# Performance work log

Hardware: AMD Instinct MI355X
Metric: run time of the kernel (lower is better)

Reference implementation:

```python
import jax, jax.numpy as jnp
import numpy as np

HEADS = 8
DIM_HEAD = 32


def setup_inputs() -> dict:
    key = jax.random.key(0)
    k1, k2, k3, k4 = jax.random.split(key, 4)
    dim, hidden = 256, HEADS * DIM_HEAD
    x = jax.random.normal(k1, (4, dim, 48, 48), dtype=jnp.float32)
    # 1x1 conv weights stored as [out_ch, in_ch]
    w_qkv = jax.random.normal(k2, (3 * hidden, dim), dtype=jnp.float32) * (dim ** -0.5)
    w_out = jax.random.normal(k3, (dim, hidden), dtype=jnp.float32) * (hidden ** -0.5)
    b_out = jax.random.normal(k4, (dim,), dtype=jnp.float32) * 0.01
    return {"x": x, "w_qkv": w_qkv, "w_out": w_out, "b_out": b_out}


def reference(x, w_qkv, w_out, b_out):
    B, C, H, W = x.shape
    n = H * W
    scale = DIM_HEAD ** -0.5
    # 1x1 conv QKV projection: [B, 3*hidden, H, W] -> [B, 3, heads, dh, n]
    qkv = jnp.einsum('oc,bchw->bohw', w_qkv, x).reshape(B, 3, HEADS, DIM_HEAD, n)
    q, k, v = qkv[:, 0], qkv[:, 1], qkv[:, 2]  # each [B, h, dh, n]
    sim = jnp.einsum('bhdi,bhdj->bhij', q, k) * scale  # [B, h, n, n]
    attn = jax.nn.softmax(sim, axis=-1)
    out = jnp.einsum('bhij,bhdj->bhdi', attn, v)  # [B, h, dh, n] -> channels (h d)
    out = out.reshape(B, HEADS * DIM_HEAD, H, W)
    return jnp.einsum('oc,bchw->bohw', w_out, out) + b_out[None, :, None, None]
```

## Files before the change

### kernel.cpp

```cpp
#include <hip/hip_runtime.h>
#include <hip/hip_bf16.h>

#define NSP 2304
#define NB  4

typedef unsigned short u16;
typedef __attribute__((ext_vector_type(8))) short short8;
typedef __attribute__((ext_vector_type(4))) float f32x4;
typedef __attribute__((ext_vector_type(4))) unsigned short u16x4;

#define K1S 0.25508040852656425f

static __device__ inline u16 f2bf(float f) {
  return __builtin_bit_cast(unsigned short, __float2bfloat16(f));
}
static __device__ inline unsigned cvtpk(float a, float b) {
  unsigned r;
  asm("v_cvt_pk_bf16_f32 %0, %1, %2" : "=v"(r) : "v"(a), "v"(b));
  return r;
}

__global__ __launch_bounds__(256) void convert_w(
    const float* __restrict__ wq, const float* __restrict__ wo,
    u16* __restrict__ dst) {
  int i = (blockIdx.x * 256 + threadIdx.x) * 4;
  float4 v;
  if (i < 196608) v = *(const float4*)(wq + i);
  else            v = *(const float4*)(wo + (i - 196608));
  u16x4 p = {f2bf(v.x), f2bf(v.y), f2bf(v.z), f2bf(v.w)};
  *(u16x4*)(dst + i) = p;
}

__global__ __launch_bounds__(256) void transpose_x(
    const float* __restrict__ x, u16* __restrict__ xT) {
  __shared__ float tile[32][33];
  const int t = threadIdx.x;
  const int n0 = blockIdx.x * 32, c0 = blockIdx.y * 32, b = blockIdx.z;
  const float* xb = x + ((size_t)b * 256 + c0) * NSP + n0;
#pragma unroll
  for (int e = t; e < 1024; e += 256) {
    int cc = e >> 5, nn = e & 31;
    tile[cc][nn] = xb[(size_t)cc * NSP + nn];
  }
  __syncthreads();
  u16* xTb = xT + ((size_t)b * NSP + n0) * 256 + c0;
#pragma unroll
  for (int e = t; e < 1024; e += 256) {
    int nn = e >> 5, cc = e & 31;
    xTb[(size_t)nn * 256 + cc] = f2bf(tile[cc][nn]);
  }
}

template <int EPI>
__global__ __launch_bounds__(256) void gemm_mfma(
    const u16* __restrict__ A, const u16* __restrict__ B,
    u16* __restrict__ qkT, u16* __restrict__ vbuf,
    float* __restrict__ outf, const float* __restrict__ bias, int N) {
  __shared__ u16 As[64][264];
  __shared__ u16 Bs[64][264];
  const int t = threadIdx.x, lane = t & 63, wid = t >> 6;
  const int lo = lane & 15, g = lane >> 4;
  const int wr = wid >> 1, wc = wid & 1;
  const int row0 = blockIdx.y * 64, col0 = blockIdx.x * 64, b = blockIdx.z;

  const int sr = t >> 2, c4 = t & 3;
  const u16* Arow = A + (size_t)(row0 + sr) * 256;
  const u16* Brow = B + ((size_t)b * N + col0 + sr) * 256;
#pragma unroll
  for (int i = 0; i < 8; ++i) {
    int col = (c4 + 4 * i) * 8;
    *(uint4*)&As[sr][col] = *(const uint4*)&Arow[col];
    *(uint4*)&Bs[sr][col] = *(const uint4*)&Brow[col];
  }
  __syncthreads();

  f32x4 acc[2][2];
#pragma unroll
  for (int i = 0; i < 2; ++i)
#pragma unroll
    for (int j = 0; j < 2; ++j) acc[i][j] = (f32x4){0, 0, 0, 0};

  const int ar0 = wr * 32 + lo, br0 = wc * 32 + lo;
#pragma unroll
  for (int kk = 0; kk < 8; ++kk) {
    int kc = kk * 32 + g * 8;
    short8 a0 = *(const short8*)&As[ar0][kc];
    short8 a1 = *(const short8*)&As[ar0 + 16][kc];
    short8 b0 = *(const short8*)&Bs[br0][kc];
    short8 b1 = *(const short8*)&Bs[br0 + 16][kc];
    acc[0][0] = __builtin_amdgcn_mfma_f32_16x16x32_bf16(a0, b0, acc[0][0], 0, 0, 0);
    acc[0][1] = __builtin_amdgcn_mfma_f32_16x16x32_bf16(a0, b1, acc[0][1], 0, 0, 0);
    acc[1][0] = __builtin_amdgcn_mfma_f32_16x16x32_bf16(a1, b0, acc[1][0], 0, 0, 0);
    acc[1][1] = __builtin_amdgcn_mfma_f32_16x16x32_bf16(a1, b1, acc[1][1], 0, 0, 0);
  }

  const float qs = (EPI == 0 && row0 < 256) ? K1S : 1.0f;
#pragma unroll
  for (int m2 = 0; m2 < 2; ++m2)
#pragma unroll
    for (int n2 = 0; n2 < 2; ++n2) {
      int m = row0 + wr * 32 + m2 * 16 + g * 4;
      int n = col0 + wc * 32 + n2 * 16 + lo;
      if constexpr (EPI == 0) {
        if (row0 < 512) {
          u16x4 pk = {f2bf(acc[m2][n2][0] * qs), f2bf(acc[m2][n2][1] * qs),
                      f2bf(acc[m2][n2][2] * qs), f2bf(acc[m2][n2][3] * qs)};
          *(u16x4*)(qkT + ((size_t)b * NSP + n) * 512 + m) = pk;
        } else {
#pragma unroll
          for (int r = 0; r < 4; ++r)
            vbuf[((size_t)b * 256 + (m - 512 + r)) * NSP + n] =
                f2bf(acc[m2][n2][r]);
        }
      } else {
#pragma unroll
        for (int r = 0; r < 4; ++r)
          outf[((size_t)b * 256 + m + r) * NSP + n] =
              acc[m2][n2][r] + bias[m + r];
      }
    }
}

__global__ __launch_bounds__(128, 2) void attn_mfma(
    const u16* __restrict__ qkT, const u16* __restrict__ vbuf,
    float* __restrict__ part) {
  const int jb = blockIdx.x;
  const int h  = jb & 7;
  const int q2 = jb >> 3;
  const int kp = q2 & 1;
  const int q3 = q2 >> 1;
  const int it = q3 % 24;
  const int b  = q3 / 24;
  const int grp = q3 * 8 + h;
  const int t = threadIdx.x, lane = t & 63, w = t >> 6;
  const int lo = lane & 15, g = lane >> 4;
  const int i0 = it * 96;
  const int j0base = kp * 1152;

  const u16* qkTb = qkT + (size_t)b * NSP * 512;
  const u16* vb   = vbuf + ((size_t)b * 256 + h * 32) * NSP;

  __shared__ u16 Kt[2][64][40];
  __shared__ u16 Vs[2][32][70];

  short8 qf[3];
#pragma unroll
  for (int qh = 0; qh < 3; ++qh)
    qf[qh] = *(const short8*)(qkTb +
              (size_t)(i0 + w * 48 + qh * 16 + lo) * 512 + h * 32 + g * 8);

  const int kr = t >> 2, kpd = (t & 3) * 8;
  const int vr = t >> 3, vjp = (t & 7) * 8;
  const int pc0 = (vjp & ~31) | (8 * ((vjp >> 2) & 3) + 4 * ((vjp >> 4) & 1));
  const u16* ksrc = qkTb + 256 + h * 32 + kpd;
  const u16* vsrc = vb + (size_t)vr * NSP + vjp;

  uint4 kv[2], vv[2];
  kv[0] = *(const uint4*)(ksrc + (size_t)(j0base + kr) * 512);
  kv[1] = *(const uint4*)(ksrc + (size_t)(j0base + kr + 32) * 512);
  vv[0] = *(const uint4*)(vsrc + j0base);
  vv[1] = *(const uint4*)(vsrc + j0base + (size_t)16 * NSP);
  *(uint4*)&Kt[0][kr][kpd]      = kv[0];
  *(uint4*)&Kt[0][kr + 32][kpd] = kv[1];
  *(uint2*)&Vs[0][vr][pc0]           = make_uint2(vv[0].x, vv[0].y);
  *(uint2*)&Vs[0][vr][pc0 + 8]       = make_uint2(vv[0].z, vv[0].w);
  *(uint2*)&Vs[0][vr + 16][pc0]      = make_uint2(vv[1].x, vv[1].y);
  *(uint2*)&Vs[0][vr + 16][pc0 + 8]  = make_uint2(vv[1].z, vv[1].w);
  __syncthreads();

  short8 ones;
#pragma unroll
  for (int e = 0; e < 8; ++e) ones[e] = (short)0x3F80;

  f32x4 a0[3], a1[3], al[3];
#pragma unroll
  for (int qh = 0; qh < 3; ++qh) {
    a0[qh] = (f32x4){0, 0, 0, 0};
    a1[qh] = (f32x4){0, 0, 0, 0};
    al[qh] = (f32x4){0, 0, 0, 0};
  }

  for (int s = 0; s < 18; ++s) {
    const int cur = s & 1;
    if (s + 1 < 18) {
      const int j0n = j0base + (s + 1) * 64;
      kv[0] = *(const uint4*)(ksrc + (size_t)(j0n + kr) * 512);
      kv[1] = *(const uint4*)(ksrc + (size_t)(j0n + kr + 32) * 512);
      vv[0] = *(const uint4*)(vsrc + j0n);
      vv[1] = *(const uint4*)(vsrc + j0n + (size_t)16 * NSP);
    }

    short8 kf0 = *(const short8*)&Kt[cur][lo][g * 8];
    short8 kf1 = *(const short8*)&Kt[cur][16 + lo][g * 8];
    short8 kf2 = *(const short8*)&Kt[cur][32 + lo][g * 8];
    short8 kf3 = *(const short8*)&Kt[cur][48 + lo][g * 8];
    short8 vf00 = *(const short8*)&Vs[cur][lo][8 * g];
    short8 vf01 = *(const short8*)&Vs[cur][lo][32 + 8 * g];
    short8 vf10 = *(const short8*)&Vs[cur][16 + lo][8 * g];
    short8 vf11 = *(const short8*)&Vs[cur][16 + lo][32 + 8 * g];

#pragma unroll
    for (int qh = 0; qh < 3; ++qh) {
      __builtin_amdgcn_s_setprio(1);
      f32x4 sv0 = __builtin_amdgcn_mfma_f32_16x16x32_bf16(kf0, qf[qh], (f32x4){0,0,0,0}, 0, 0, 0);
      f32x4 sv1 = __builtin_amdgcn_mfma_f32_16x16x32_bf16(kf1, qf[qh], (f32x4){0,0,0,0}, 0, 0, 0);
      f32x4 sv2 = __builtin_amdgcn_mfma_f32_16x16x32_bf16(kf2, qf[qh], (f32x4){0,0,0,0}, 0, 0, 0);
      f32x4 sv3 = __builtin_amdgcn_mfma_f32_16x16x32_bf16(kf3, qf[qh], (f32x4){0,0,0,0}, 0, 0, 0);
      __builtin_amdgcn_s_setprio(0);

      f32x4 e0, e1, e2, e3;
#pragma unroll
      for (int r = 0; r < 4; ++r) {
        e0[r] = __builtin_amdgcn_exp2f(sv0[r]);
        e1[r] = __builtin_amdgcn_exp2f(sv1[r]);
        e2[r] = __builtin_amdgcn_exp2f(sv2[r]);
        e3[r] = __builtin_amdgcn_exp2f(sv3[r]);
      }
      uint4 P0 = {cvtpk(e0[0], e0[1]), cvtpk(e0[2], e0[3]),
                  cvtpk(e1[0], e1[1]), cvtpk(e1[2], e1[3])};
      uint4 P1 = {cvtpk(e2[0], e2[1]), cvtpk(e2[2], e2[3]),
                  cvtpk(e3[0], e3[1]), cvtpk(e3[2], e3[3])};
      short8 pf0 = __builtin_bit_cast(short8, P0);
      short8 pf1 = __builtin_bit_cast(short8, P1);

      __builtin_amdgcn_s_setprio(1);
      a0[qh] = __builtin_amdgcn_mfma_f32_16x16x32_bf16(pf0, vf00, a0[qh], 0, 0, 0);
      a1[qh] = __builtin_amdgcn_mfma_f32_16x16x32_bf16(pf0, vf10, a1[qh], 0, 0, 0);
      al[qh] = __builtin_amdgcn_mfma_f32_16x16x32_bf16(pf0, ones, al[qh], 0, 0, 0);
      a0[qh] = __builtin_amdgcn_mfma_f32_16x16x32_bf16(pf1, vf01, a0[qh], 0, 0, 0);
      a1[qh] = __builtin_amdgcn_mfma_f32_16x16x32_bf16(pf1, vf11, a1[qh], 0, 0, 0);
      al[qh] = __builtin_amdgcn_mfma_f32_16x16x32_bf16(pf1, ones, al[qh], 0, 0, 0);
      __builtin_amdgcn_s_setprio(0);
    }

    if (s + 1 < 18) {
      *(uint4*)&Kt[cur ^ 1][kr][kpd]      = kv[0];
      *(uint4*)&Kt[cur ^ 1][kr + 32][kpd] = kv[1];
      *(uint2*)&Vs[cur ^ 1][vr][pc0]          = make_uint2(vv[0].x, vv[0].y);
      *(uint2*)&Vs[cur ^ 1][vr][pc0 + 8]      = make_uint2(vv[0].z, vv[0].w);
      *(uint2*)&Vs[cur ^ 1][vr + 16][pc0]     = make_uint2(vv[1].x, vv[1].y);
      *(uint2*)&Vs[cur ^ 1][vr + 16][pc0 + 8] = make_uint2(vv[1].z, vv[1].w);
    }
    __syncthreads();
  }

  float* pg = part + ((size_t)kp * 768 + grp) * (33 * 96);
#pragma unroll
  for (int qh = 0; qh < 3; ++qh) {
    int row = w * 48 + qh * 16 + g * 4;
    *(f32x4*)&pg[(size_t)lo * 96 + row]        = a0[qh];
    *(f32x4*)&pg[(size_t)(16 + lo) * 96 + row] = a1[qh];
    if (lo == 0) *(f32x4*)&pg[(size_t)32 * 96 + row] = al[qh];
  }
}

__global__ __launch_bounds__(128) void merge_attn(
    const float* __restrict__ part, u16* __restrict__ attnoT) {
  const int grp = blockIdx.x;
  const int h = grp & 7, q3 = grp >> 3;
  const int it = q3 % 24, b = q3 / 24;
  const int t = threadIdx.x;
  if (t >= 96) return;
  const float* p0 = part + (size_t)grp * (33 * 96);
  const float* p1 = part + ((size_t)768 + grp) * (33 * 96);
  float inv = 1.0f / (p0[32 * 96 + t] + p1[32 * 96 + t]);
  u16* ob = attnoT + ((size_t)b * NSP + it * 96 + t) * 256 + h * 32;
#pragma unroll
  for (int c4 = 0; c4 < 8; ++c4) {
    u16x4 o;
#pragma unroll
    for (int j = 0; j < 4; ++j) {
      int c = c4 * 4 + j;
      o[j] = f2bf((p0[c * 96 + t] + p1[c * 96 + t]) * inv);
    }
    *(u16x4*)&ob[c4 * 4] = o;
  }
}

extern "C" void kernel_launch(void* const* d_in, const int* in_sizes, int n_in,
                              void* d_out, int out_size, void* d_ws, size_t ws_size,
                              hipStream_t stream) {
  const float* x     = (const float*)d_in[0];
  const float* w_qkv = (const float*)d_in[1];
  const float* w_out = (const float*)d_in[2];
  const float* b_out = (const float*)d_in[3];
  float* out = (float*)d_out;

  u16* wbf    = (u16*)d_ws;
  u16* xT     = wbf + 262144;
  u16* qkT    = xT + (size_t)NB * NSP * 256;
  u16* vbuf   = qkT + (size_t)NB * NSP * 512;
  u16* attnoT = vbuf + (size_t)NB * 256 * NSP;
  float* part = (float*)(attnoT + (size_t)NB * NSP * 256);

  dim3 blk(256);
  convert_w<<<256, blk, 0, stream>>>(w_qkv, w_out, wbf);
  transpose_x<<<dim3(NSP / 32, 8, NB), blk, 0, stream>>>(x, xT);
  gemm_mfma<0><<<dim3(NSP / 64, 12, NB), blk, 0, stream>>>(
      wbf, xT, qkT, vbuf, nullptr, nullptr, NSP);
  attn_mfma<<<dim3(1536), dim3(128), 0, stream>>>(qkT, vbuf, part);
  merge_attn<<<dim3(768), dim3(128), 0, stream>>>(part, attnoT);
  gemm_mfma<1><<<dim3(NSP / 64, 4, NB), blk, 0, stream>>>(
      wbf + 196608, attnoT, nullptr, nullptr, out, b_out, NSP);
}
```

Baseline: 75.45 us.

## Fuse weight conversion into transpose and re-split attention into 4 key chunks

Folds the weight bf16 conversion into the x-transpose kernel as an extra column of blocks, removing one launch. The attention kernel moves to 256-thread blocks of 4 waves covering 192 queries, with the key range split into 4 partitions of 576 instead of 2 of 1152. Each thread now stages one K and one V chunk per step, and the merge kernel sums 4 partials. This trades more partial-sum traffic in the merge for larger blocks, higher occupancy bounds and shorter per-block loops.

```diff
diff --git a/kernel.cpp b/kernel.cpp
--- a/kernel.cpp
+++ b/kernel.cpp
@@ -20,21 +20,26 @@
   return r;
 }
 
-__global__ __launch_bounds__(256) void convert_w(
-    const float* __restrict__ wq, const float* __restrict__ wo,
-    u16* __restrict__ dst) {
-  int i = (blockIdx.x * 256 + threadIdx.x) * 4;
-  float4 v;
-  if (i < 196608) v = *(const float4*)(wq + i);
-  else            v = *(const float4*)(wo + (i - 196608));
-  u16x4 p = {f2bf(v.x), f2bf(v.y), f2bf(v.z), f2bf(v.w)};
-  *(u16x4*)(dst + i) = p;
-}
-
-__global__ __launch_bounds__(256) void transpose_x(
-    const float* __restrict__ x, u16* __restrict__ xT) {
+__global__ __launch_bounds__(256) void prep_fused(
+    const float* __restrict__ x, const float* __restrict__ wq,
+    const float* __restrict__ wo, u16* __restrict__ xT,
+    u16* __restrict__ wbf) {
+  const int t = threadIdx.x;
+  if (blockIdx.x == 72) {
+    const int cid = blockIdx.y * 4 + blockIdx.z;
+    const int base = cid * 8192;
+#pragma unroll
+    for (int i = 0; i < 8; ++i) {
+      int idx = base + (i * 256 + t) * 4;
+      float4 v;
+      if (idx < 196608) v = *(const float4*)(wq + idx);
+      else              v = *(const float4*)(wo + (idx - 196608));
+      u16x4 p = {f2bf(v.x), f2bf(v.y), f2bf(v.z), f2bf(v.w)};
+      *(u16x4*)(wbf + idx) = p;
+    }
+    return;
+  }
   __shared__ float tile[32][33];
-  const int t = threadIdx.x;
   const int n0 = blockIdx.x * 32, c0 = blockIdx.y * 32, b = blockIdx.z;
   const float* xb = x + ((size_t)b * 256 + c0) * NSP + n0;
 #pragma unroll
@@ -121,21 +126,21 @@
     }
 }
 
-__global__ __launch_bounds__(128, 2) void attn_mfma(
+__global__ __launch_bounds__(256, 6) void attn_mfma(
     const u16* __restrict__ qkT, const u16* __restrict__ vbuf,
     float* __restrict__ part) {
   const int jb = blockIdx.x;
   const int h  = jb & 7;
   const int q2 = jb >> 3;
-  const int kp = q2 & 1;
-  const int q3 = q2 >> 1;
-  const int it = q3 % 24;
-  const int b  = q3 / 24;
+  const int kp = q2 & 3;
+  const int q3 = q2 >> 2;
+  const int it = q3 % 12;
+  const int b  = q3 / 12;
   const int grp = q3 * 8 + h;
   const int t = threadIdx.x, lane = t & 63, w = t >> 6;
   const int lo = lane & 15, g = lane >> 4;
-  const int i0 = it * 96;
-  const int j0base = kp * 1152;
+  const int i0 = it * 192;
+  const int j0base = kp * 576;
 
   const u16* qkTb = qkT + (size_t)b * NSP * 512;
   const u16* vb   = vbuf + ((size_t)b * 256 + h * 32) * NSP;
@@ -155,17 +160,11 @@
   const u16* ksrc = qkTb + 256 + h * 32 + kpd;
   const u16* vsrc = vb + (size_t)vr * NSP + vjp;
 
-  uint4 kv[2], vv[2];
-  kv[0] = *(const uint4*)(ksrc + (size_t)(j0base + kr) * 512);
-  kv[1] = *(const uint4*)(ksrc + (size_t)(j0base + kr + 32) * 512);
-  vv[0] = *(const uint4*)(vsrc + j0base);
-  vv[1] = *(const uint4*)(vsrc + j0base + (size_t)16 * NSP);
-  *(uint4*)&Kt[0][kr][kpd]      = kv[0];
-  *(uint4*)&Kt[0][kr + 32][kpd] = kv[1];
-  *(uint2*)&Vs[0][vr][pc0]           = make_uint2(vv[0].x, vv[0].y);
-  *(uint2*)&Vs[0][vr][pc0 + 8]       = make_uint2(vv[0].z, vv[0].w);
-  *(uint2*)&Vs[0][vr + 16][pc0]      = make_uint2(vv[1].x, vv[1].y);
-  *(uint2*)&Vs[0][vr + 16][pc0 + 8]  = make_uint2(vv[1].z, vv[1].w);
+  uint4 kv = *(const uint4*)(ksrc + (size_t)(j0base + kr) * 512);
+  uint4 vv = *(const uint4*)(vsrc + j0base);
+  *(uint4*)&Kt[0][kr][kpd] = kv;
+  *(uint2*)&Vs[0][vr][pc0]     = make_uint2(vv.x, vv.y);
+  *(uint2*)&Vs[0][vr][pc0 + 8] = make_uint2(vv.z, vv.w);
   __syncthreads();
 
   short8 ones;
@@ -180,14 +179,12 @@
     al[qh] = (f32x4){0, 0, 0, 0};
   }
 
-  for (int s = 0; s < 18; ++s) {
+  for (int s = 0; s < 9; ++s) {
     const int cur = s & 1;
-    if (s + 1 < 18) {
+    if (s + 1 < 9) {
       const int j0n = j0base + (s + 1) * 64;
-      kv[0] = *(const uint4*)(ksrc + (size_t)(j0n + kr) * 512);
-      kv[1] = *(const uint4*)(ksrc + (size_t)(j0n + kr + 32) * 512);
-      vv[0] = *(const uint4*)(vsrc + j0n);
-      vv[1] = *(const uint4*)(vsrc + j0n + (size_t)16 * NSP);
+      kv = *(const uint4*)(ksrc + (size_t)(j0n + kr) * 512);
+      vv = *(const uint4*)(vsrc + j0n);
     }
 
     short8 kf0 = *(const short8*)&Kt[cur][lo][g * 8];
@@ -233,45 +230,47 @@
       __builtin_amdgcn_s_setprio(0);
     }
 
-    if (s + 1 < 18) {
-      *(uint4*)&Kt[cur ^ 1][kr][kpd]      = kv[0];
-      *(uint4*)&Kt[cur ^ 1][kr + 32][kpd] = kv[1];
-      *(uint2*)&Vs[cur ^ 1][vr][pc0]          = make_uint2(vv[0].x, vv[0].y);
-      *(uint2*)&Vs[cur ^ 1][vr][pc0 + 8]      = make_uint2(vv[0].z, vv[0].w);
-      *(uint2*)&Vs[cur ^ 1][vr + 16][pc0]     = make_uint2(vv[1].x, vv[1].y);
-      *(uint2*)&Vs[cur ^ 1][vr + 16][pc0 + 8] = make_uint2(vv[1].z, vv[1].w);
+    if (s + 1 < 9) {
+      *(uint4*)&Kt[cur ^ 1][kr][kpd] = kv;
+      *(uint2*)&Vs[cur ^ 1][vr][pc0]     = make_uint2(vv.x, vv.y);
+      *(uint2*)&Vs[cur ^ 1][vr][pc0 + 8] = make_uint2(vv.z, vv.w);
     }
     __syncthreads();
   }
 
-  float* pg = part + ((size_t)kp * 768 + grp) * (33 * 96);
+  float* pg = part + ((size_t)(kp * 384 + grp)) * (33 * 192);
 #pragma unroll
   for (int qh = 0; qh < 3; ++qh) {
     int row = w * 48 + qh * 16 + g * 4;
-    *(f32x4*)&pg[(size_t)lo * 96 + row]        = a0[qh];
-    *(f32x4*)&pg[(size_t)(16 + lo) * 96 + row] = a1[qh];
-    if (lo == 0) *(f32x4*)&pg[(size_t)32 * 96 + row] = al[qh];
-  }
-}
-
-__global__ __launch_bounds__(128) void merge_attn(
+    *(f32x4*)&pg[(size_t)lo * 192 + row]        = a0[qh];
+    *(f32x4*)&pg[(size_t)(16 + lo) * 192 + row] = a1[qh];
+    if (lo == 0) *(f32x4*)&pg[(size_t)32 * 192 + row] = al[qh];
+  }
+}
+
+__global__ __launch_bounds__(192) void merge_attn(
     const float* __restrict__ part, u16* __restrict__ attnoT) {
   const int grp = blockIdx.x;
   const int h = grp & 7, q3 = grp >> 3;
-  const int it = q3 % 24, b = q3 / 24;
+  const int it = q3 % 12, b = q3 / 12;
   const int t = threadIdx.x;
-  if (t >= 96) return;
-  const float* p0 = part + (size_t)grp * (33 * 96);
-  const float* p1 = part + ((size_t)768 + grp) * (33 * 96);
-  float inv = 1.0f / (p0[32 * 96 + t] + p1[32 * 96 + t]);
-  u16* ob = attnoT + ((size_t)b * NSP + it * 96 + t) * 256 + h * 32;
+  const float* p0 = part + (size_t)grp * (33 * 192);
+  const size_t stride = (size_t)384 * 33 * 192;
+  float lsum = 0.0f;
+#pragma unroll
+  for (int kp = 0; kp < 4; ++kp) lsum += p0[kp * stride + 32 * 192 + t];
+  float inv = 1.0f / lsum;
+  u16* ob = attnoT + ((size_t)b * NSP + it * 192 + t) * 256 + h * 32;
 #pragma unroll
   for (int c4 = 0; c4 < 8; ++c4) {
     u16x4 o;
 #pragma unroll
     for (int j = 0; j < 4; ++j) {
       int c = c4 * 4 + j;
-      o[j] = f2bf((p0[c * 96 + t] + p1[c * 96 + t]) * inv);
+      float v = 0.0f;
+#pragma unroll
+      for (int kp = 0; kp < 4; ++kp) v += p0[kp * stride + c * 192 + t];
+      o[j] = f2bf(v * inv);
     }
     *(u16x4*)&ob[c4 * 4] = o;
   }
@@ -294,12 +293,11 @@
   float* part = (float*)(attnoT + (size_t)NB * NSP * 256);
 
   dim3 blk(256);
-  convert_w<<<256, blk, 0, stream>>>(w_qkv, w_out, wbf);
-  transpose_x<<<dim3(NSP / 32, 8, NB), blk, 0, stream>>>(x, xT);
+  prep_fused<<<dim3(73, 8, NB), blk, 0, stream>>>(x, w_qkv, w_out, xT, wbf);
   gemm_mfma<0><<<dim3(NSP / 64, 12, NB), blk, 0, stream>>>(
       wbf, xT, qkT, vbuf, nullptr, nullptr, NSP);
-  attn_mfma<<<dim3(1536), dim3(128), 0, stream>>>(qkT, vbuf, part);
-  merge_attn<<<dim3(768), dim3(128), 0, stream>>>(part, attnoT);
+  attn_mfma<<<dim3(1536), blk, 0, stream>>>(qkT, vbuf, part);
+  merge_attn<<<dim3(384), dim3(192), 0, stream>>>(part, attnoT);
   gemm_mfma<1><<<dim3(NSP / 64, 4, NB), blk, 0, stream>>>(
       wbf + 196608, attnoT, nullptr, nullptr, out, b_out, NSP);
 }
```

Result: slower. 169.4 us (+124.6%).
